# Kernel optimization log

Measured on AMD Instinct MI355X. Metric: run time of the kernel, lower is better.

Reference implementation:

```python
import jax, jax.numpy as jnp
import numpy as np

M, N, D, P = 1024, 4096, 128, 2048
H = N // D  # 32
L = 4096   # cache length


def setup_inputs() -> dict:
    key = jax.random.key(0)
    ks = jax.random.split(key, 6)
    # scales keep the naive (non max-subtracted) exp-softmax in fp32 range
    X = jax.random.normal(ks[0], (M, N), dtype=jnp.float32) * 0.5
    W_q = jax.random.normal(ks[1], (N, N), dtype=jnp.float32) * 0.01
    W_k = jax.random.normal(ks[2], (N, N), dtype=jnp.float32) * 0.01
    W_v = jax.random.normal(ks[3], (N, N), dtype=jnp.float32) * 0.01
    cache_K = jax.random.normal(ks[4], (H, L, D), dtype=jnp.float32) * 0.1
    cache_V = jax.random.normal(ks[5], (H, L, D), dtype=jnp.float32) * 0.1
    return {"X": X, "W_q": W_q, "W_k": W_k, "W_v": W_v,
            "cache_K": cache_K, "cache_V": cache_V}


def reference(X, W_q, W_k, W_v, cache_K, cache_V):
    # fused QKV projection: [M, N] @ [N, 3N]
    W_qkv = jnp.concatenate([W_q, W_k, W_v], axis=1)
    qkv = X @ W_qkv
    q, k, v = jnp.split(qkv, 3, axis=-1)
    q = q.reshape(M, H, D).transpose(1, 0, 2)  # [H, M, D]
    k = k.reshape(M, H, D).transpose(1, 0, 2)  # [H, M, D]
    v = v.reshape(M, H, D).transpose(1, 0, 2)  # [H, M, D]
    # KV-cache write at position P
    k_cache = jax.lax.dynamic_update_slice(cache_K, k, (0, P, 0))  # [H, L, D]
    v_cache = jax.lax.dynamic_update_slice(cache_V, v, (0, P, 0))
    # naive (no max-subtraction) exp softmax attention over the full cache
    scores = jnp.einsum('hmd,hld->hml', q, k_cache)  # [H, M, L]
    scores_exp = jnp.exp(scores)
    weights = scores_exp / jnp.sum(scores_exp, axis=-1, keepdims=True)
    output = jnp.einsum('hml,hld->hmd', weights, v_cache)  # [H, M, D]
    return output.transpose(1, 0, 2).reshape(M, H * D)
```

## Files before the change

kernel.cpp:

```cpp
#include <hip/hip_runtime.h>

#define MM 1024
#define NN 4096
#define DD 128
#define HH 32
#define LL 4096
#define PP 2048

typedef __attribute__((ext_vector_type(8))) short short8;
typedef __attribute__((ext_vector_type(4))) float f32x4;

__device__ __forceinline__ ushort f2bf(float f) {
  unsigned u = __builtin_bit_cast(unsigned, f);
  u += 0x7fffu + ((u >> 16) & 1u);
  return (ushort)(u >> 16);
}

__device__ __forceinline__ void gl_lds16(const void* g, void* l) {
  __builtin_amdgcn_global_load_lds(
      (const __attribute__((address_space(1))) void*)g,
      (__attribute__((address_space(3))) void*)l, 16, 0, 0);
}

__global__ __launch_bounds__(256) void convert_kernel(
    const float* __restrict__ src, ushort* __restrict__ dst, int n8) {
  int i = blockIdx.x * 256 + threadIdx.x;
  if (i >= n8) return;
  const float4* s = (const float4*)src + (size_t)i * 2;
  float4 a = s[0], b = s[1];
  union { ushort s[8]; uint4 v; } pk;
  pk.s[0] = f2bf(a.x); pk.s[1] = f2bf(a.y);
  pk.s[2] = f2bf(a.z); pk.s[3] = f2bf(a.w);
  pk.s[4] = f2bf(b.x); pk.s[5] = f2bf(b.y);
  pk.s[6] = f2bf(b.z); pk.s[7] = f2bf(b.w);
  ((uint4*)dst)[i] = pk.v;
}

__global__ __launch_bounds__(256) void transpose_w_kernel(
    const float* __restrict__ W0, const float* __restrict__ W1,
    const float* __restrict__ W2, ushort* __restrict__ Wt) {
  __shared__ __align__(16) ushort tile[64][72];
  int z = blockIdx.z;
  const float* W = (z == 0) ? W0 : ((z == 1) ? W1 : W2);
  ushort* out = Wt + (size_t)z * NN * NN;
  int r0 = blockIdx.x * 64, c0 = blockIdx.y * 64;
  int t = threadIdx.x;
#pragma unroll
  for (int i = 0; i < 4; ++i) {
    int c = i * 256 + t;
    int r = c >> 4, cc = (c & 15) * 4;
    float4 v = *(const float4*)(W + (size_t)(r0 + r) * NN + c0 + cc);
    tile[r][cc + 0] = f2bf(v.x);
    tile[r][cc + 1] = f2bf(v.y);
    tile[r][cc + 2] = f2bf(v.z);
    tile[r][cc + 3] = f2bf(v.w);
  }
  __syncthreads();
#pragma unroll
  for (int i = 0; i < 2; ++i) {
    int c = i * 256 + t;
    int j = c >> 3, kk = (c & 7) * 8;
    union { ushort s[8]; uint4 v; } pk;
#pragma unroll
    for (int u = 0; u < 8; ++u) pk.s[u] = tile[kk + u][j];
    *(uint4*)(out + (size_t)(c0 + j) * NN + r0 + kk) = pk.v;
  }
}

__global__ __launch_bounds__(256) void transpose_v_kernel(
    const float* __restrict__ cacheV, const ushort* __restrict__ v_new,
    ushort* __restrict__ Vt) {
  __shared__ __align__(16) ushort tile[64][72];
  int l0 = blockIdx.x * 64, d0 = blockIdx.y * 64, h = blockIdx.z;
  int t = threadIdx.x;
  bool isnew = (l0 >= PP && l0 < PP + MM);
  if (isnew) {
    const ushort* src = v_new + (size_t)(l0 - PP) * NN + h * DD + d0;
#pragma unroll
    for (int i = 0; i < 2; ++i) {
      int c = i * 256 + t;
      int r = c >> 3, cc = (c & 7) * 8;
      *(uint4*)&tile[r][cc] = *(const uint4*)(src + (size_t)r * NN + cc);
    }
  } else {
    const float* src = cacheV + ((size_t)h * LL + l0) * DD + d0;
#pragma unroll
    for (int i = 0; i < 4; ++i) {
      int c = i * 256 + t;
      int r = c >> 4, cc = (c & 15) * 4;
      float4 v = *(const float4*)(src + (size_t)r * DD + cc);
      tile[r][cc + 0] = f2bf(v.x);
      tile[r][cc + 1] = f2bf(v.y);
      tile[r][cc + 2] = f2bf(v.z);
      tile[r][cc + 3] = f2bf(v.w);
    }
  }
  __syncthreads();
#pragma unroll
  for (int i = 0; i < 2; ++i) {
    int c = i * 256 + t;
    int j = c >> 3, kk = (c & 7) * 8;
    union { ushort s[8]; uint4 v; } pk;
#pragma unroll
    for (int u = 0; u < 8; ++u) pk.s[u] = tile[kk + u][j];
    *(uint4*)(Vt + ((size_t)(h * DD + d0 + j)) * LL + l0 + kk) = pk.v;
  }
}

__global__ __launch_bounds__(256) void qkv_gemm_kernel(
    const ushort* __restrict__ X, const ushort* __restrict__ Wt,
    ushort* __restrict__ q_ws, ushort* __restrict__ k_ws,
    ushort* __restrict__ v_ws) {
  __shared__ __align__(16) ushort Alds[128 * 64];
  __shared__ __align__(16) ushort Blds[128 * 64];
  int t = threadIdx.x;
  int lane = t & 63, quad = lane >> 4, l15 = lane & 15;
  int wv = t >> 6, wm = wv >> 1, wn = wv & 1;
  int m0 = blockIdx.x * 128;
  int wsel = blockIdx.y >> 5;
  int col0 = (blockIdx.y & 31) * 128;
  const ushort* Wsrc = Wt + (size_t)wsel * NN * NN + (size_t)col0 * NN;
  ushort* dst = (wsel == 0) ? q_ws : ((wsel == 1) ? k_ws : v_ws);

  int wuni = __builtin_amdgcn_readfirstlane(t & 192);

  const ushort* aG[4];
  const ushort* bG[4];
  unsigned ldsb[4];
#pragma unroll
  for (int i = 0; i < 4; ++i) {
    int c = i * 256 + t;
    int row = c >> 3, g = (c & 7) ^ (row & 7);
    aG[i] = X + (size_t)(m0 + row) * NN + g * 8;
    bG[i] = Wsrc + (size_t)row * NN + g * 8;
    ldsb[i] = (unsigned)(i * 256 + wuni) * 16u;
  }
  unsigned aAddr[4][2], bAddr[4][2];
#pragma unroll
  for (int mb = 0; mb < 4; ++mb)
#pragma unroll
    for (int s = 0; s < 2; ++s) {
      int row = wm * 64 + mb * 16 + l15;
      int g = s * 4 + quad;
      aAddr[mb][s] = (unsigned)(row * 128 + ((g ^ (row & 7)) * 16));
    }
#pragma unroll
  for (int nb = 0; nb < 4; ++nb)
#pragma unroll
    for (int s = 0; s < 2; ++s) {
      int row = wn * 64 + nb * 16 + l15;
      int g = s * 4 + quad;
      bAddr[nb][s] = (unsigned)(row * 128 + ((g ^ (row & 7)) * 16));
    }

  f32x4 acc[4][4];
#pragma unroll
  for (int mb = 0; mb < 4; ++mb)
#pragma unroll
    for (int nb = 0; nb < 4; ++nb) acc[mb][nb] = (f32x4){0.f, 0.f, 0.f, 0.f};

  for (int kt = 0; kt < 64; ++kt) {
#pragma unroll
    for (int i = 0; i < 4; ++i) gl_lds16(aG[i], (char*)Alds + ldsb[i]);
#pragma unroll
    for (int i = 0; i < 4; ++i) gl_lds16(bG[i], (char*)Blds + ldsb[i]);
#pragma unroll
    for (int i = 0; i < 4; ++i) { aG[i] += 64; bG[i] += 64; }
    __syncthreads();
#pragma unroll
    for (int s = 0; s < 2; ++s) {
      short8 af[4], bf[4];
#pragma unroll
      for (int mb = 0; mb < 4; ++mb)
        af[mb] = *(const short8*)((const char*)Alds + aAddr[mb][s]);
#pragma unroll
      for (int nb = 0; nb < 4; ++nb)
        bf[nb] = *(const short8*)((const char*)Blds + bAddr[nb][s]);
#pragma unroll
      for (int mb = 0; mb < 4; ++mb)
#pragma unroll
        for (int nb = 0; nb < 4; ++nb)
          acc[mb][nb] = __builtin_amdgcn_mfma_f32_16x16x32_bf16(
              af[mb], bf[nb], acc[mb][nb], 0, 0, 0);
    }
    __syncthreads();
  }

#pragma unroll
  for (int mb = 0; mb < 4; ++mb)
#pragma unroll
    for (int nb = 0; nb < 4; ++nb)
#pragma unroll
      for (int r = 0; r < 4; ++r) {
        int row = m0 + wm * 64 + mb * 16 + quad * 4 + r;
        int col = col0 + wn * 64 + nb * 16 + l15;
        dst[(size_t)row * NN + col] = f2bf(acc[mb][nb][r]);
      }
}

__global__ __launch_bounds__(256, 2) void attn_kernel(
    const ushort* __restrict__ q_ws, const ushort* __restrict__ k_ws,
    const ushort* __restrict__ Kb, const ushort* __restrict__ Vt,
    float* __restrict__ out) {
  __shared__ __align__(16) char smem[35840];
  ushort* Plds = (ushort*)smem;
  float* denlds = (float*)(smem + 34816);
  float* Olds = (float*)smem;

  int t = threadIdx.x;
  int lane = t & 63, quad = lane >> 4, l15 = lane & 15;
  int wv = t >> 6;
  int quad8 = quad * 8, quad4 = quad * 4, wv16 = wv * 16;
  int wv16l15 = wv16 + l15;
  int flat = (int)(blockIdx.y * 16 + blockIdx.x);
  int swz = ((flat & 7) << 6) | (flat >> 3);
  int m0 = (swz & 15) * 64;
  int h = swz >> 4;

  short8 qf[4][4];
#pragma unroll
  for (int mb = 0; mb < 4; ++mb) {
    const ushort* qr =
        q_ws + (size_t)(m0 + mb * 16 + l15) * NN + h * DD + quad8;
#pragma unroll
    for (int ds = 0; ds < 4; ++ds) qf[mb][ds] = *(const short8*)(qr + ds * 32);
  }

  const ushort* vrow = Vt + ((size_t)(h * DD + wv * 32 + l15)) * LL;
  const ushort* vrow16 = vrow + (size_t)16 * LL;

  f32x4 Oacc[2][4];
#pragma unroll
  for (int db = 0; db < 2; ++db)
#pragma unroll
    for (int mb = 0; mb < 4; ++mb) Oacc[db][mb] = (f32x4){0.f, 0.f, 0.f, 0.f};
  float denp[4][4];
#pragma unroll
  for (int mb = 0; mb < 4; ++mb)
#pragma unroll
    for (int r = 0; r < 4; ++r) denp[mb][r] = 0.f;

  short8 kra[4], krb[4], vra[2][2], vrb[2][2];

  {
    const ushort* kp = Kb + ((size_t)h * LL + wv16l15) * DD;
    kra[0] = *(const short8*)(kp + quad8);
    kra[1] = *(const short8*)(kp + 32 + quad8);
    kra[2] = *(const short8*)(kp + 64 + quad8);
    kra[3] = *(const short8*)(kp + 96 + quad8);
    vra[0][0] = *(const short8*)(vrow + quad8);
    vra[0][1] = *(const short8*)(vrow + 32 + quad8);
    vra[1][0] = *(const short8*)(vrow16 + quad8);
    vra[1][1] = *(const short8*)(vrow16 + 32 + quad8);
  }

#define ATTN_STEP(LT, KC, VC, KN, VN, PF)                                      \
  do {                                                                         \
    if (PF) {          \
      int l0n = ((LT) + 1) << 6;                                               \
      size_t krow = (size_t)l0n + (size_t)wv16l15;                             \
      const ushort* kp = (l0n >= PP && l0n < PP + MM)                          \
                             ? k_ws + (krow - PP) * NN + h * DD                \
                             : Kb + ((size_t)h * LL + krow) * DD;              \
      KN[0] = *(const short8*)(kp + quad8);                                    \
      KN[1] = *(const short8*)(kp + 32 + quad8);                               \
      KN[2] = *(const short8*)(kp + 64 + quad8);                               \
      KN[3] = *(const short8*)(kp + 96 + quad8);                               \
      const ushort* vp0 = vrow + l0n;                                          \
      const ushort* vp1 = vrow16 + l0n;                                        \
      VN[0][0] = *(const short8*)(vp0 + quad8);                                \
      VN[0][1] = *(const short8*)(vp0 + 32 + quad8);                           \
      VN[1][0] = *(const short8*)(vp1 + quad8);                                \
      VN[1][1] = *(const short8*)(vp1 + 32 + quad8);                           \
    }                                                                          \
      \
    f32x4 sac[4];                                                              \
    __builtin_amdgcn_s_setprio(1);                                             \
    _Pragma("unroll") for (int mb = 0; mb < 4; ++mb) {                         \
      f32x4 s = (f32x4){0.f, 0.f, 0.f, 0.f};                                   \
      s = __builtin_amdgcn_mfma_f32_16x16x32_bf16(qf[mb][0], KC[0], s, 0, 0, 0);\
      s = __builtin_amdgcn_mfma_f32_16x16x32_bf16(qf[mb][1], KC[1], s, 0, 0, 0);\
      s = __builtin_amdgcn_mfma_f32_16x16x32_bf16(qf[mb][2], KC[2], s, 0, 0, 0);\
      s = __builtin_amdgcn_mfma_f32_16x16x32_bf16(qf[mb][3], KC[3], s, 0, 0, 0);\
      sac[mb] = s;                                                             \
    }                                                                          \
    __builtin_amdgcn_s_setprio(0);                                             \
    _Pragma("unroll") for (int mb = 0; mb < 4; ++mb) {                         \
      float e0 = __expf(sac[mb][0]), e1 = __expf(sac[mb][1]);                  \
      float e2 = __expf(sac[mb][2]), e3 = __expf(sac[mb][3]);                  \
      denp[mb][0] += e0; denp[mb][1] += e1;                                    \
      denp[mb][2] += e2; denp[mb][3] += e3;                                    \
      ushort* pw = Plds + (mb * 16 + quad4) * 72 + wv16l15;                    \
      pw[0] = f2bf(e0); pw[72] = f2bf(e1);                                     \
      pw[144] = f2bf(e2); pw[216] = f2bf(e3);                                  \
    }                                                                          \
    asm volatile("s_waitcnt lgkmcnt(0)" ::: "memory");                         \
    __builtin_amdgcn_s_barrier();     \
          \
    __builtin_amdgcn_s_setprio(1);                                             \
    _Pragma("unroll") for (int mb = 0; mb < 4; ++mb) {                         \
      const ushort* pr = Plds + (mb * 16 + l15) * 72 + quad8;                  \
      short8 p0 = *(const short8*)pr;                                          \
      short8 p1 = *(const short8*)(pr + 32);                                   \
      Oacc[0][mb] = __builtin_amdgcn_mfma_f32_16x16x32_bf16(VC[0][0], p0,      \
                                                            Oacc[0][mb], 0, 0, 0);\
      Oacc[0][mb] = __builtin_amdgcn_mfma_f32_16x16x32_bf16(VC[0][1], p1,      \
                                                            Oacc[0][mb], 0, 0, 0);\
      Oacc[1][mb] = __builtin_amdgcn_mfma_f32_16x16x32_bf16(VC[1][0], p0,      \
                                                            Oacc[1][mb], 0, 0, 0);\
      Oacc[1][mb] = __builtin_amdgcn_mfma_f32_16x16x32_bf16(VC[1][1], p1,      \
                                                            Oacc[1][mb], 0, 0, 0);\
    }                                                                          \
    __builtin_amdgcn_s_setprio(0);                                             \
    asm volatile("s_waitcnt lgkmcnt(0)" ::: "memory");                         \
    __builtin_amdgcn_s_barrier();   \
  } while (0)

  for (int i = 0; i < 31; ++i) {
    ATTN_STEP(2 * i, kra, vra, krb, vrb, 1);
    ATTN_STEP(2 * i + 1, krb, vrb, kra, vra, 1);
  }
  ATTN_STEP(62, kra, vra, krb, vrb, 1);
  ATTN_STEP(63, krb, vrb, kra, vra, 0);
#undef ATTN_STEP

#pragma unroll
  for (int mb = 0; mb < 4; ++mb)
#pragma unroll
    for (int r = 0; r < 4; ++r) {
      float v = denp[mb][r];
      v += __shfl_xor(v, 1);
      v += __shfl_xor(v, 2);
      v += __shfl_xor(v, 4);
      v += __shfl_xor(v, 8);
      denp[mb][r] = v;
    }
  if (l15 == 0) {
#pragma unroll
    for (int mb = 0; mb < 4; ++mb)
#pragma unroll
      for (int r = 0; r < 4; ++r)
        denlds[wv * 64 + mb * 16 + quad4 + r] = denp[mb][r];
  }
  __syncthreads();

#pragma unroll
  for (int mb = 0; mb < 4; ++mb) {
    int m = mb * 16 + l15;
    float den =
        denlds[m] + denlds[64 + m] + denlds[128 + m] + denlds[192 + m];
    float inv = 1.0f / den;
#pragma unroll
    for (int db = 0; db < 2; ++db)
#pragma unroll
      for (int r = 0; r < 4; ++r) {
        int d = wv * 32 + db * 16 + quad4 + r;
        Olds[m * 136 + d] = Oacc[db][mb][r] * inv;
      }
  }
  __syncthreads();
  {
    int m = t >> 2, c0 = (t & 3) * 32;
    float* orow = out + (size_t)(m0 + m) * NN + h * DD + c0;
#pragma unroll
    for (int j = 0; j < 32; j += 4) {
      float4 v;
      v.x = Olds[m * 136 + c0 + j + 0];
      v.y = Olds[m * 136 + c0 + j + 1];
      v.z = Olds[m * 136 + c0 + j + 2];
      v.w = Olds[m * 136 + c0 + j + 3];
      *(float4*)(orow + j) = v;
    }
  }
}

extern "C" void kernel_launch(void* const* d_in, const int* in_sizes, int n_in,
                              void* d_out, int out_size, void* d_ws,
                              size_t ws_size, hipStream_t stream) {
  const float* X = (const float*)d_in[0];
  const float* Wq = (const float*)d_in[1];
  const float* Wk = (const float*)d_in[2];
  const float* Wv = (const float*)d_in[3];
  const float* cK = (const float*)d_in[4];
  const float* cV = (const float*)d_in[5];
  float* out = (float*)d_out;
  char* wsb = (char*)d_ws;

  ushort* Wt = (ushort*)wsb;
  ushort* Kb = (ushort*)wsb;
  ushort* Vt = (ushort*)(wsb + 33554432);
  ushort* Xb = (ushort*)(wsb + 100663296);
  ushort* q_ws = (ushort*)(wsb + 109051904);
  ushort* k_ws = (ushort*)(wsb + 117440512);
  ushort* v_ws = (ushort*)(wsb + 125829120);

  convert_kernel<<<2048, 256, 0, stream>>>(X, Xb, MM * NN / 8);
  transpose_w_kernel<<<dim3(64, 64, 3), 256, 0, stream>>>(Wq, Wk, Wv, Wt);
  qkv_gemm_kernel<<<dim3(8, 96), 256, 0, stream>>>(Xb, Wt, q_ws, k_ws, v_ws);
  convert_kernel<<<8192, 256, 0, stream>>>(cK, Kb, HH * LL * DD / 8);
  transpose_v_kernel<<<dim3(64, 2, 32), 256, 0, stream>>>(cV, v_ws, Vt);
  attn_kernel<<<dim3(16, 32), 256, 0, stream>>>(q_ws, k_ws, Kb, Vt, out);
}
```

Baseline: 579.5 us.

## Halve attention query tile, double-buffer P in LDS, drop second barrier

Shrinks each attention block from 64 to 32 query rows and doubles the grid to 1024 blocks, with launch bounds raised to 4 blocks per CU and LDS halved. The P tile is double-buffered, which removes the second barrier per step. Scores are computed transposed (K as the A operand), so exp values pack with v_cvt_pk_bf16 into a single 8-byte LDS store, and the denominator reduction across lanes shrinks. V loads move from a one-step-ahead prefetch to the start of each step, and K/V are now re-read twice as often across blocks. Latency hiding therefore relies more on occupancy.

```diff
diff --git a/kernel.cpp b/kernel.cpp
--- a/kernel.cpp
+++ b/kernel.cpp
@@ -198,157 +198,152 @@
       }
 }
 
-__global__ __launch_bounds__(256, 2) void attn_kernel(
+__global__ __launch_bounds__(256, 4) void attn_kernel(
     const ushort* __restrict__ q_ws, const ushort* __restrict__ k_ws,
     const ushort* __restrict__ Kb, const ushort* __restrict__ Vt,
     float* __restrict__ out) {
-  __shared__ __align__(16) char smem[35840];
-  ushort* Plds = (ushort*)smem;
-  float* denlds = (float*)(smem + 34816);
+  __shared__ __align__(16) char smem[17920];
+  float* denlds = (float*)(smem + 17408);
   float* Olds = (float*)smem;
 
   int t = threadIdx.x;
   int lane = t & 63, quad = lane >> 4, l15 = lane & 15;
   int wv = t >> 6;
-  int quad8 = quad * 8, quad4 = quad * 4, wv16 = wv * 16;
+  int quad8 = quad * 8, quad4 = quad * 4, quad16 = quad * 16;
+  int wv16 = wv * 16;
   int wv16l15 = wv16 + l15;
-  int flat = (int)(blockIdx.y * 16 + blockIdx.x);
-  int swz = ((flat & 7) << 6) | (flat >> 3);
-  int m0 = (swz & 15) * 64;
-  int h = swz >> 4;
-
-  short8 qf[4][4];
-#pragma unroll
-  for (int mb = 0; mb < 4; ++mb) {
+  int flat = (int)(blockIdx.y * 32 + blockIdx.x);
+  int swz = ((flat & 7) << 7) | (flat >> 3);
+  int m0 = (swz & 31) * 32;
+  int h = swz >> 5;
+
+  short8 qf[2][4];
+#pragma unroll
+  for (int mb = 0; mb < 2; ++mb) {
     const ushort* qr =
         q_ws + (size_t)(m0 + mb * 16 + l15) * NN + h * DD + quad8;
 #pragma unroll
     for (int ds = 0; ds < 4; ++ds) qf[mb][ds] = *(const short8*)(qr + ds * 32);
   }
 
+  const ushort* kbK = Kb + ((size_t)h * LL + wv16l15) * DD;
+  const ushort* kbW = k_ws + (size_t)wv16l15 * NN + h * DD;
   const ushort* vrow = Vt + ((size_t)(h * DD + wv * 32 + l15)) * LL;
   const ushort* vrow16 = vrow + (size_t)16 * LL;
 
-  f32x4 Oacc[2][4];
+  f32x4 Oacc[2][2];
 #pragma unroll
   for (int db = 0; db < 2; ++db)
 #pragma unroll
-    for (int mb = 0; mb < 4; ++mb) Oacc[db][mb] = (f32x4){0.f, 0.f, 0.f, 0.f};
-  float denp[4][4];
-#pragma unroll
-  for (int mb = 0; mb < 4; ++mb)
-#pragma unroll
-    for (int r = 0; r < 4; ++r) denp[mb][r] = 0.f;
-
-  short8 kra[4], krb[4], vra[2][2], vrb[2][2];
-
-  {
-    const ushort* kp = Kb + ((size_t)h * LL + wv16l15) * DD;
-    kra[0] = *(const short8*)(kp + quad8);
-    kra[1] = *(const short8*)(kp + 32 + quad8);
-    kra[2] = *(const short8*)(kp + 64 + quad8);
-    kra[3] = *(const short8*)(kp + 96 + quad8);
-    vra[0][0] = *(const short8*)(vrow + quad8);
-    vra[0][1] = *(const short8*)(vrow + 32 + quad8);
-    vra[1][0] = *(const short8*)(vrow16 + quad8);
-    vra[1][1] = *(const short8*)(vrow16 + 32 + quad8);
-  }
-
-#define ATTN_STEP(LT, KC, VC, KN, VN, PF)                                      \
+    for (int mb = 0; mb < 2; ++mb) Oacc[db][mb] = (f32x4){0.f, 0.f, 0.f, 0.f};
+  float denp0 = 0.f, denp1 = 0.f;
+
+  short8 kra[4], krb[4], vc[2][2];
+
+  kra[0] = *(const short8*)(kbK + quad8);
+  kra[1] = *(const short8*)(kbK + 32 + quad8);
+  kra[2] = *(const short8*)(kbK + 64 + quad8);
+  kra[3] = *(const short8*)(kbK + 96 + quad8);
+
+#define ATTN_STEP(LT, KC, KN, PF)                                              \
   do {                                                                         \
-    if (PF) {          \
-      int l0n = ((LT) + 1) << 6;                                               \
-      size_t krow = (size_t)l0n + (size_t)wv16l15;                             \
+    const int l0c = (LT) << 6;                                                 \
+    const unsigned pb = (((LT) & 1) ? 4608u : 0u);                             \
+        \
+    vc[0][0] = *(const short8*)(vrow + l0c + quad8);                           \
+    vc[0][1] = *(const short8*)(vrow + l0c + 32 + quad8);                      \
+    vc[1][0] = *(const short8*)(vrow16 + l0c + quad8);                         \
+    vc[1][1] = *(const short8*)(vrow16 + l0c + 32 + quad8);                    \
+    if (PF) {       \
+      const int l0n = ((LT) + 1) << 6;                                         \
       const ushort* kp = (l0n >= PP && l0n < PP + MM)                          \
-                             ? k_ws + (krow - PP) * NN + h * DD                \
-                             : Kb + ((size_t)h * LL + krow) * DD;              \
+                             ? kbW + (size_t)(l0n - PP) * NN                   \
+                             : kbK + (size_t)l0n * DD;                         \
       KN[0] = *(const short8*)(kp + quad8);                                    \
       KN[1] = *(const short8*)(kp + 32 + quad8);                               \
       KN[2] = *(const short8*)(kp + 64 + quad8);                               \
       KN[3] = *(const short8*)(kp + 96 + quad8);                               \
-      const ushort* vp0 = vrow + l0n;                                          \
-      const ushort* vp1 = vrow16 + l0n;                                        \
-      VN[0][0] = *(const short8*)(vp0 + quad8);                                \
-      VN[0][1] = *(const short8*)(vp0 + 32 + quad8);                           \
-      VN[1][0] = *(const short8*)(vp1 + quad8);                                \
-      VN[1][1] = *(const short8*)(vp1 + 32 + quad8);                           \
     }                                                                          \
-      \
-    f32x4 sac[4];                                                              \
+    \
+    f32x4 s0 = (f32x4){0.f, 0.f, 0.f, 0.f};                                    \
+    f32x4 s1 = (f32x4){0.f, 0.f, 0.f, 0.f};                                    \
     __builtin_amdgcn_s_setprio(1);                                             \
-    _Pragma("unroll") for (int mb = 0; mb < 4; ++mb) {                         \
-      f32x4 s = (f32x4){0.f, 0.f, 0.f, 0.f};                                   \
-      s = __builtin_amdgcn_mfma_f32_16x16x32_bf16(qf[mb][0], KC[0], s, 0, 0, 0);\
-      s = __builtin_amdgcn_mfma_f32_16x16x32_bf16(qf[mb][1], KC[1], s, 0, 0, 0);\
-      s = __builtin_amdgcn_mfma_f32_16x16x32_bf16(qf[mb][2], KC[2], s, 0, 0, 0);\
-      s = __builtin_amdgcn_mfma_f32_16x16x32_bf16(qf[mb][3], KC[3], s, 0, 0, 0);\
-      sac[mb] = s;                                                             \
-    }                                                                          \
+    s0 = __builtin_amdgcn_mfma_f32_16x16x32_bf16(KC[0], qf[0][0], s0, 0, 0, 0);\
+    s1 = __builtin_amdgcn_mfma_f32_16x16x32_bf16(KC[0], qf[1][0], s1, 0, 0, 0);\
+    s0 = __builtin_amdgcn_mfma_f32_16x16x32_bf16(KC[1], qf[0][1], s0, 0, 0, 0);\
+    s1 = __builtin_amdgcn_mfma_f32_16x16x32_bf16(KC[1], qf[1][1], s1, 0, 0, 0);\
+    s0 = __builtin_amdgcn_mfma_f32_16x16x32_bf16(KC[2], qf[0][2], s0, 0, 0, 0);\
+    s1 = __builtin_amdgcn_mfma_f32_16x16x32_bf16(KC[2], qf[1][2], s1, 0, 0, 0);\
+    s0 = __builtin_amdgcn_mfma_f32_16x16x32_bf16(KC[3], qf[0][3], s0, 0, 0, 0);\
+    s1 = __builtin_amdgcn_mfma_f32_16x16x32_bf16(KC[3], qf[1][3], s1, 0, 0, 0);\
     __builtin_amdgcn_s_setprio(0);                                             \
-    _Pragma("unroll") for (int mb = 0; mb < 4; ++mb) {                         \
-      float e0 = __expf(sac[mb][0]), e1 = __expf(sac[mb][1]);                  \
-      float e2 = __expf(sac[mb][2]), e3 = __expf(sac[mb][3]);                  \
-      denp[mb][0] += e0; denp[mb][1] += e1;                                    \
-      denp[mb][2] += e2; denp[mb][3] += e3;                                    \
-      ushort* pw = Plds + (mb * 16 + quad4) * 72 + wv16l15;                    \
-      pw[0] = f2bf(e0); pw[72] = f2bf(e1);                                     \
-      pw[144] = f2bf(e2); pw[216] = f2bf(e3);                                  \
+    {             \
+      float e0 = __expf(s0[0]), e1 = __expf(s0[1]);                            \
+      float e2 = __expf(s0[2]), e3 = __expf(s0[3]);                            \
+      denp0 += (e0 + e1) + (e2 + e3);                                          \
+      unsigned w0, w1;                                                         \
+      asm("v_cvt_pk_bf16_f32 %0, %1, %2" : "=v"(w0) : "v"(e0), "v"(e1));       \
+      asm("v_cvt_pk_bf16_f32 %0, %1, %2" : "=v"(w1) : "v"(e2), "v"(e3));       \
+      uint2 pw; pw.x = w0; pw.y = w1;                                          \
+      *(uint2*)(smem + pb + (unsigned)l15 * 144u + (unsigned)(wv16 * 2) +      \
+                (unsigned)quad8) = pw;                                         \
+      float f0 = __expf(s1[0]), f1 = __expf(s1[1]);                            \
+      float f2 = __expf(s1[2]), f3 = __expf(s1[3]);                            \
+      denp1 += (f0 + f1) + (f2 + f3);                                          \
+      unsigned w2, w3;                                                         \
+      asm("v_cvt_pk_bf16_f32 %0, %1, %2" : "=v"(w2) : "v"(f0), "v"(f1));       \
+      asm("v_cvt_pk_bf16_f32 %0, %1, %2" : "=v"(w3) : "v"(f2), "v"(f3));       \
+      uint2 pw2; pw2.x = w2; pw2.y = w3;                                       \
+      *(uint2*)(smem + pb + (unsigned)(16 + l15) * 144u +                      \
+                (unsigned)(wv16 * 2) + (unsigned)quad8) = pw2;                 \
     }                                                                          \
     asm volatile("s_waitcnt lgkmcnt(0)" ::: "memory");                         \
     __builtin_amdgcn_s_barrier();     \
-          \
+    asm volatile("" ::: "memory");                                             \
+                   \
     __builtin_amdgcn_s_setprio(1);                                             \
-    _Pragma("unroll") for (int mb = 0; mb < 4; ++mb) {                         \
-      const ushort* pr = Plds + (mb * 16 + l15) * 72 + quad8;                  \
-      short8 p0 = *(const short8*)pr;                                          \
-      short8 p1 = *(const short8*)(pr + 32);                                   \
-      Oacc[0][mb] = __builtin_amdgcn_mfma_f32_16x16x32_bf16(VC[0][0], p0,      \
-                                                            Oacc[0][mb], 0, 0, 0);\
-      Oacc[0][mb] = __builtin_amdgcn_mfma_f32_16x16x32_bf16(VC[0][1], p1,      \
-                                                            Oacc[0][mb], 0, 0, 0);\
-      Oacc[1][mb] = __builtin_amdgcn_mfma_f32_16x16x32_bf16(VC[1][0], p0,      \
-                                                            Oacc[1][mb], 0, 0, 0);\
-      Oacc[1][mb] = __builtin_amdgcn_mfma_f32_16x16x32_bf16(VC[1][1], p1,      \
-                                                            Oacc[1][mb], 0, 0, 0);\
+    _Pragma("unroll") for (int mb = 0; mb < 2; ++mb) {                         \
+      const char* pr = smem + pb + (unsigned)(mb * 16 + l15) * 144u;           \
+      short8 p0 = *(const short8*)(pr + quad16);                               \
+      short8 p1 = *(const short8*)(pr + 64 + quad16);                          \
+      Oacc[0][mb] = __builtin_amdgcn_mfma_f32_16x16x32_bf16(                   \
+          vc[0][0], p0, Oacc[0][mb], 0, 0, 0);                                 \
+      Oacc[0][mb] = __builtin_amdgcn_mfma_f32_16x16x32_bf16(                   \
+          vc[0][1], p1, Oacc[0][mb], 0, 0, 0);                                 \
+      Oacc[1][mb] = __builtin_amdgcn_mfma_f32_16x16x32_bf16(                   \
+          vc[1][0], p0, Oacc[1][mb], 0, 0, 0);                                 \
+      Oacc[1][mb] = __builtin_amdgcn_mfma_f32_16x16x32_bf16(                   \
+          vc[1][1], p1, Oacc[1][mb], 0, 0, 0);                                 \
     }                                                                          \
     __builtin_amdgcn_s_setprio(0);                                             \
-    asm volatile("s_waitcnt lgkmcnt(0)" ::: "memory");                         \
-    __builtin_amdgcn_s_barrier();   \
   } while (0)
 
   for (int i = 0; i < 31; ++i) {
-    ATTN_STEP(2 * i, kra, vra, krb, vrb, 1);
-    ATTN_STEP(2 * i + 1, krb, vrb, kra, vra, 1);
-  }
-  ATTN_STEP(62, kra, vra, krb, vrb, 1);
-  ATTN_STEP(63, krb, vrb, kra, vra, 0);
+    ATTN_STEP(2 * i, kra, krb, 1);
+    ATTN_STEP(2 * i + 1, krb, kra, 1);
+  }
+  ATTN_STEP(62, kra, krb, 1);
+  ATTN_STEP(63, krb, kra, 0);
 #undef ATTN_STEP
 
-#pragma unroll
-  for (int mb = 0; mb < 4; ++mb)
-#pragma unroll
-    for (int r = 0; r < 4; ++r) {
-      float v = denp[mb][r];
-      v += __shfl_xor(v, 1);
-      v += __shfl_xor(v, 2);
-      v += __shfl_xor(v, 4);
-      v += __shfl_xor(v, 8);
-      denp[mb][r] = v;
-    }
-  if (l15 == 0) {
-#pragma unroll
-    for (int mb = 0; mb < 4; ++mb)
-#pragma unroll
-      for (int r = 0; r < 4; ++r)
-        denlds[wv * 64 + mb * 16 + quad4 + r] = denp[mb][r];
+  {
+    float v0 = denp0, v1 = denp1;
+    v0 += __shfl_xor(v0, 16);
+    v0 += __shfl_xor(v0, 32);
+    v1 += __shfl_xor(v1, 16);
+    v1 += __shfl_xor(v1, 32);
+    if (quad == 0) {
+      denlds[wv * 32 + l15] = v0;
+      denlds[wv * 32 + 16 + l15] = v1;
+    }
   }
   __syncthreads();
 
 #pragma unroll
-  for (int mb = 0; mb < 4; ++mb) {
+  for (int mb = 0; mb < 2; ++mb) {
     int m = mb * 16 + l15;
     float den =
-        denlds[m] + denlds[64 + m] + denlds[128 + m] + denlds[192 + m];
+        denlds[m] + denlds[32 + m] + denlds[64 + m] + denlds[96 + m];
     float inv = 1.0f / den;
 #pragma unroll
     for (int db = 0; db < 2; ++db)
@@ -360,10 +355,10 @@
   }
   __syncthreads();
   {
-    int m = t >> 2, c0 = (t & 3) * 32;
+    int m = t >> 3, c0 = (t & 7) * 16;
     float* orow = out + (size_t)(m0 + m) * NN + h * DD + c0;
 #pragma unroll
-    for (int j = 0; j < 32; j += 4) {
+    for (int j = 0; j < 16; j += 4) {
       float4 v;
       v.x = Olds[m * 136 + c0 + j + 0];
       v.y = Olds[m * 136 + c0 + j + 1];
@@ -399,5 +394,5 @@
   qkv_gemm_kernel<<<dim3(8, 96), 256, 0, stream>>>(Xb, Wt, q_ws, k_ws, v_ws);
   convert_kernel<<<8192, 256, 0, stream>>>(cK, Kb, HH * LL * DD / 8);
   transpose_v_kernel<<<dim3(64, 2, 32), 256, 0, stream>>>(cV, v_ws, Vt);
-  attn_kernel<<<dim3(16, 32), 256, 0, stream>>>(q_ws, k_ws, Kb, Vt, out);
-}
+  attn_kernel<<<dim3(32, 32), 256, 0, stream>>>(q_ws, k_ws, Kb, Vt, out);
+}
```

Result: slower. 672.5 us (+16.0%).
